# Optimization experiments

Hardware: AMD Instinct MI355X
Metric: run time of the kernel (lower is better)

## Reference

```python
import jax, jax.numpy as jnp
import numpy as np

H = 4096          # hidden_size
NH = 32           # num query heads
NKV = 8           # num kv heads
HD = H // NH      # head_dim = 128
NE = 8            # num_experts
TOPK = 2
ROPE_THETA = 10000.0
EPS = 1e-6


def rmsnorm(x, w):
    var = jnp.mean(x * x, axis=-1, keepdims=True)
    return x * jax.lax.rsqrt(var + EPS) * w


def apply_rope_neox(x, positions):
    # x: [N, heads, HD]; neox style: rotate halves
    half = HD // 2
    inv_freq = 1.0 / (ROPE_THETA ** (jnp.arange(0, HD, 2, dtype=jnp.float32) / HD))  # [half]
    ang = positions.astype(jnp.float32)[:, None] * inv_freq[None, :]                 # [N, half]
    cos = jnp.cos(ang)[:, None, :]  # [N,1,half]
    sin = jnp.sin(ang)[:, None, :]
    x1, x2 = x[..., :half], x[..., half:]
    return jnp.concatenate([x1 * cos - x2 * sin, x2 * cos + x1 * sin], axis=-1)


def setup_inputs() -> dict:
    key = jax.random.key(0)
    ks = jax.random.split(key, 6)
    N = 2048
    return {
        "positions": jnp.arange(N, dtype=jnp.int32),
        "hidden_states": jax.random.normal(ks[0], (N, H), dtype=jnp.float32),
        "w_qkv": jax.random.normal(ks[1], (H, (NH + 2 * NKV) * HD), dtype=jnp.float32) * 0.02,
        "w_o": jax.random.normal(ks[2], (NH * HD, H), dtype=jnp.float32) * 0.02,
        "w_gate": jax.random.normal(ks[3], (H, NE), dtype=jnp.float32) * 0.02,
        "rms_w_pre": jnp.ones((H,), dtype=jnp.float32),
        "rms_w_post": jnp.ones((H,), dtype=jnp.float32),
        "expert_logits": jax.random.uniform(ks[4], (N, NE), dtype=jnp.float32),
    }


def reference(positions, hidden_states, w_qkv, w_o, w_gate, rms_w_pre, rms_w_post, expert_logits):
    N = hidden_states.shape[0]
    # pre-attention RMSNorm (residual is None branch)
    residual = hidden_states
    x = rmsnorm(hidden_states, rms_w_pre)

    qkv = x @ w_qkv
    q = qkv[:, : NH * HD].reshape(N, NH, HD)
    k = qkv[:, NH * HD : (NH + NKV) * HD].reshape(N, NKV, HD)
    v = qkv[:, (NH + NKV) * HD :].reshape(N, NKV, HD)

    q = apply_rope_neox(q, positions)
    k = apply_rope_neox(k, positions)

    # GQA causal self-attention (prefill, single sequence)
    group = NH // NKV
    k_rep = jnp.repeat(k, group, axis=1)  # [N, NH, HD]
    v_rep = jnp.repeat(v, group, axis=1)
    scale = HD ** -0.5
    scores = jnp.einsum("qhd,khd->hqk", q, k_rep) * scale  # [NH, N, N]
    causal = jnp.tril(jnp.ones((N, N), dtype=bool))
    scores = jnp.where(causal[None], scores, jnp.finfo(scores.dtype).min)
    probs = jax.nn.softmax(scores, axis=-1)
    attn_out = jnp.einsum("hqk,khd->qhd", probs, v_rep).reshape(N, NH * HD)

    output = attn_out @ w_o
    # post-attention RMSNorm with fused residual add (vLLM semantics)
    s = output + residual
    residual = s
    output = rmsnorm(s, rms_w_post)

    router_logits = output @ w_gate  # computed as in source; routing result overwritten below

    # random_routing: topk over random expert logits, renormalized
    topk_weights, topk_ids = jax.lax.top_k(expert_logits, TOPK)  # [N, TOPK]
    topk_weights = topk_weights / jnp.sum(topk_weights, axis=-1, keepdims=True)

    # permute_by_exp_ids: stable sort of flattened expert ids, gather tokens
    reorder_ids = jnp.argsort(topk_ids.reshape(-1), stable=True)  # [N*TOPK]
    permuted_output = output[reorder_ids // TOPK]                 # [N*TOPK, H]
    return permuted_output, topk_weights, topk_ids, reorder_ids
```

## Files before the change

kernel.cpp:

```cpp
#include <hip/hip_runtime.h>
#include <hip/hip_bf16.h>
#include <math.h>

#define N_TOK 2048
#define H_DIM 4096
#define NH 32
#define NKV 8
#define HD 128
#define QKV_D 6144
#define NE 8
#define TOPK 2

#define OUT_PERM 0
#define OUT_W    16777216
#define OUT_IDS  16781312
#define OUT_REO  16785408

typedef __bf16 bf16x8 __attribute__((ext_vector_type(8)));
typedef float f32x4 __attribute__((ext_vector_type(4)));

typedef __attribute__((address_space(3))) void lds_void;
typedef __attribute__((address_space(1))) const void gbl_void;

__device__ __forceinline__ void gld16(const void* g, void* l) {
    __builtin_amdgcn_global_load_lds((gbl_void*)g, (lds_void*)l, 16, 0, 0);
}

__device__ __forceinline__ unsigned short f2bf(float f) {
    union { float f; unsigned u; } v; v.f = f;
    unsigned r = v.u + 0x7fff + ((v.u >> 16) & 1);
    return (unsigned short)(r >> 16);
}
__device__ __forceinline__ unsigned pack2bf(float a, float b) {
    return (unsigned)f2bf(a) | ((unsigned)f2bf(b) << 16);
}
__device__ __forceinline__ float bf2f(unsigned short u) {
    union { unsigned u; float f; } v; v.u = ((unsigned)u) << 16;
    return v.f;
}

__global__ __launch_bounds__(256) void rmsnorm_k(const float* __restrict__ x,
                                                 const float* __restrict__ w,
                                                 float* __restrict__ yf,
                                                 unsigned short* __restrict__ yb) {
    int row = blockIdx.x;
    int tid = threadIdx.x;
    const float4* x4 = (const float4*)(x + (size_t)row * H_DIM);
    const float4* w4 = (const float4*)w;
    float4 v[4];
    float ss = 0.f;
#pragma unroll
    for (int k = 0; k < 4; ++k) {
        v[k] = x4[tid + k * 256];
        ss += v[k].x * v[k].x + v[k].y * v[k].y + v[k].z * v[k].z + v[k].w * v[k].w;
    }
#pragma unroll
    for (int off = 32; off; off >>= 1) ss += __shfl_xor(ss, off);
    __shared__ float sacc[4];
    if ((tid & 63) == 0) sacc[tid >> 6] = ss;
    __syncthreads();
    float tot = sacc[0] + sacc[1] + sacc[2] + sacc[3];
    float sc = rsqrtf(tot * (1.0f / H_DIM) + 1e-6f);
#pragma unroll
    for (int k = 0; k < 4; ++k) {
        float4 ww = w4[tid + k * 256];
        float4 o;
        o.x = v[k].x * sc * ww.x;
        o.y = v[k].y * sc * ww.y;
        o.z = v[k].z * sc * ww.z;
        o.w = v[k].w * sc * ww.w;
        if (yf) {
            *(float4*)(yf + (size_t)row * H_DIM + (tid + k * 256) * 4) = o;
        } else {
            uint2 p;
            p.x = pack2bf(o.x, o.y);
            p.y = pack2bf(o.z, o.w);
            *(uint2*)(yb + (size_t)row * H_DIM + (tid + k * 256) * 4) = p;
        }
    }
}

__global__ __launch_bounds__(256) void convT_k(const float* __restrict__ src,
                                               unsigned short* __restrict__ dst,
                                               int R, int C) {
    __shared__ float t[64][68];
    int r0 = blockIdx.y * 64, c0 = blockIdx.x * 64;
    int tid = threadIdx.x;
    int lr = tid >> 4, lc = tid & 15;
#pragma unroll
    for (int it = 0; it < 4; ++it) {
        int r = lr + it * 16;
        float4 v = *(const float4*)(src + (size_t)(r0 + r) * C + c0 + lc * 4);
        *(float4*)&t[r][lc * 4] = v;
    }
    __syncthreads();
#pragma unroll
    for (int it = 0; it < 4; ++it) {
        int cc = lr + it * 16;
        uint2 o;
        o.x = pack2bf(t[lc * 4 + 0][cc], t[lc * 4 + 1][cc]);
        o.y = pack2bf(t[lc * 4 + 2][cc], t[lc * 4 + 3][cc]);
        *(uint2*)(dst + (size_t)(c0 + cc) * R + r0 + lc * 4) = o;
    }
}

__global__ __launch_bounds__(256) void gemm_k(const __hip_bfloat16* __restrict__ A,
                                              const __hip_bfloat16* __restrict__ Bt,
                                              float* __restrict__ C,
                                              unsigned short* __restrict__ Cb,
                                              const float* __restrict__ residual,
                                              int Ncols) {
    __shared__ __align__(16) __hip_bfloat16 As[2][128 * 64];
    __shared__ __align__(16) __hip_bfloat16 Bs[2][128 * 64];
    const int K = H_DIM;
    int tid = threadIdx.x, w = tid >> 6, lane = tid & 63;
    int quad = lane >> 4, l15 = lane & 15;

    int gx = gridDim.x;
    int nwg = gx * gridDim.y;
    int v = blockIdx.y * gx + blockIdx.x;
    int lin = (v & 7) * (nwg >> 3) + (v >> 3);
    int m0 = (lin % gx) * 128, n0 = (lin / gx) * 128;
    int wm = (w & 1) * 64, wn = (w >> 1) * 64;

    int rowInChunk = lane >> 3;
    int uIdx = lane & 7;
    const char* Ag[4]; const char* Bg[4];
    int chOff[4];
#pragma unroll
    for (int c = 0; c < 4; ++c) {
        int ch = w * 4 + c;
        int r = ch * 8 + rowInChunk;
        int gu = uIdx ^ (r & 7);
        Ag[c] = (const char*)(A + (size_t)(m0 + r) * K) + gu * 16;
        Bg[c] = (const char*)(Bt + (size_t)(n0 + r) * K) + gu * 16;
        chOff[c] = ch * 1024;
    }

    f32x4 acc[4][4];
#pragma unroll
    for (int i = 0; i < 4; ++i)
#pragma unroll
        for (int j = 0; j < 4; ++j) acc[i][j] = (f32x4){0.f, 0.f, 0.f, 0.f};

    const int nsteps = K / 64;

#pragma unroll
    for (int c = 0; c < 4; ++c) gld16(Ag[c], (char*)&As[0][0] + chOff[c]);
#pragma unroll
    for (int c = 0; c < 4; ++c) gld16(Bg[c], (char*)&Bs[0][0] + chOff[c]);

    for (int t = 0; t < nsteps; ++t) {
        int cur = t & 1;
        if (t + 1 < nsteps) {
            size_t kb = (size_t)(t + 1) * 128;
            char* dA = (char*)&As[cur ^ 1][0];
            char* dB = (char*)&Bs[cur ^ 1][0];
#pragma unroll
            for (int c = 0; c < 4; ++c) gld16(Ag[c] + kb, dA + chOff[c]);
#pragma unroll
            for (int c = 0; c < 4; ++c) gld16(Bg[c] + kb, dB + chOff[c]);
            asm volatile("s_waitcnt vmcnt(8)" ::: "memory");
        } else {
            asm volatile("s_waitcnt vmcnt(0)" ::: "memory");
        }
        __builtin_amdgcn_sched_barrier(0);
        __builtin_amdgcn_s_barrier();
        __builtin_amdgcn_sched_barrier(0);

        const char* sA = (const char*)&As[cur][0];
        const char* sB = (const char*)&Bs[cur][0];
#pragma unroll
        for (int kk = 0; kk < 2; ++kk) {
            bf16x8 af[4], bfr[4];
#pragma unroll
            for (int mt = 0; mt < 4; ++mt) {
                int m = wm + mt * 16 + l15;
                af[mt] = *(const bf16x8*)(sA + m * 128 + (((kk * 4 + quad) ^ (m & 7)) * 16));
            }
#pragma unroll
            for (int nt = 0; nt < 4; ++nt) {
                int n = wn + nt * 16 + l15;
                bfr[nt] = *(const bf16x8*)(sB + n * 128 + (((kk * 4 + quad) ^ (n & 7)) * 16));
            }
#pragma unroll
            for (int mt = 0; mt < 4; ++mt)
#pragma unroll
                for (int nt = 0; nt < 4; ++nt)
                    acc[mt][nt] = __builtin_amdgcn_mfma_f32_16x16x32_bf16(af[mt], bfr[nt], acc[mt][nt], 0, 0, 0);
        }
        __builtin_amdgcn_sched_barrier(0);
        __builtin_amdgcn_s_barrier();
        __builtin_amdgcn_sched_barrier(0);
    }
#pragma unroll
    for (int mt = 0; mt < 4; ++mt)
#pragma unroll
        for (int nt = 0; nt < 4; ++nt)
#pragma unroll
            for (int r = 0; r < 4; ++r) {
                int row = m0 + wm + mt * 16 + quad * 4 + r;
                int col = n0 + wn + nt * 16 + l15;
                size_t off = (size_t)row * Ncols + col;
                float vv = acc[mt][nt][r];
                if (Cb) {
                    Cb[off] = f2bf(vv);
                } else {
                    if (residual) vv += residual[off];
                    C[off] = vv;
                }
            }
}

__global__ __launch_bounds__(512) void gemm8_k(const __hip_bfloat16* __restrict__ A,
                                               const __hip_bfloat16* __restrict__ Bt,
                                               unsigned short* __restrict__ Cb,
                                               int Ncols) {
    __shared__ __align__(16) __hip_bfloat16 As[2][256 * 64];
    __shared__ __align__(16) __hip_bfloat16 Bs[2][256 * 64];
    const int K = H_DIM;
    int tid = threadIdx.x, w = tid >> 6, lane = tid & 63;
    int quad = lane >> 4, l15 = lane & 15;
    int wr = w >> 2, wc = w & 3;

    int gx = gridDim.x;
    int nwg = gx * gridDim.y;
    int v = blockIdx.y * gx + blockIdx.x;
    int lin = (v & 7) * (nwg >> 3) + (v >> 3);
    int m0 = (lin % gx) * 256, n0 = (lin / gx) * 256;

    const char* Abase = (const char*)A + (size_t)m0 * (K * 2);
    const char* Bbase = (const char*)Bt + (size_t)n0 * (K * 2);
    int srow = w * 8 + (lane >> 3);

    auto stage = [&](const char* gbase, int rowoff, char* lbase, size_t kbyte) {
#pragma unroll
        for (int l = 0; l < 2; ++l) {
            int r = l * 64 + srow;
            int gu = (lane & 7) ^ (r & 7);
            gld16(gbase + (size_t)(rowoff + r) * (K * 2) + kbyte + gu * 16,
                  lbase + (l * 64 + w * 8) * 128);
        }
    };

    f32x4 acc[8][4];
#pragma unroll
    for (int i = 0; i < 8; ++i)
#pragma unroll
        for (int j = 0; j < 4; ++j) acc[i][j] = (f32x4){0.f, 0.f, 0.f, 0.f};

    const int ntiles = K / 64;

    stage(Abase, 0,   (char*)&As[0][0],         0);
    stage(Abase, 128, (char*)&As[0][0] + 16384, 0);
    stage(Bbase, 0,   (char*)&Bs[0][0],         0);
    stage(Bbase, 128, (char*)&Bs[0][0] + 16384, 0);
    stage(Bbase, 0,   (char*)&Bs[1][0],         128);
    stage(Bbase, 128, (char*)&Bs[1][0] + 16384, 128);
    asm volatile("s_waitcnt vmcnt(4)" ::: "memory");
    __builtin_amdgcn_sched_barrier(0);
    __builtin_amdgcn_s_barrier();
    __builtin_amdgcn_sched_barrier(0);

    for (int j = 0; j < ntiles; ++j) {
        int d = j & 1;
        const char* sA = (const char*)&As[d][0];
        const char* sB = (const char*)&Bs[d][0];
        char* nA = (char*)&As[d ^ 1][0];
        char* pB = (char*)&Bs[d][0];
        size_t kb1 = (size_t)(j + 1) * 128, kb2 = (size_t)(j + 2) * 128;
        bf16x8 aR[4][2], bR[4][2];

#pragma unroll
        for (int mt = 0; mt < 4; ++mt)
#pragma unroll
            for (int kk = 0; kk < 2; ++kk) {
                int m = wr * 128 + mt * 16 + l15;
                aR[mt][kk] = *(const bf16x8*)(sA + m * 128 + (((kk * 4 + quad) ^ (m & 7)) * 16));
            }
#pragma unroll
        for (int nt = 0; nt < 2; ++nt)
#pragma unroll
            for (int kk = 0; kk < 2; ++kk) {
                int n = wc * 64 + nt * 16 + l15;
                bR[nt][kk] = *(const bf16x8*)(sB + n * 128 + (((kk * 4 + quad) ^ (n & 7)) * 16));
            }
        if (j + 1 < ntiles) stage(Abase, 0, nA, kb1);
        __builtin_amdgcn_sched_barrier(0);
        __builtin_amdgcn_s_barrier();
        asm volatile("s_waitcnt lgkmcnt(0)" ::: "memory");
        __builtin_amdgcn_sched_barrier(0);
        __builtin_amdgcn_s_setprio(1);
#pragma unroll
        for (int mt = 0; mt < 4; ++mt)
#pragma unroll
            for (int nt = 0; nt < 2; ++nt)
#pragma unroll
                for (int kk = 0; kk < 2; ++kk)
                    acc[mt][nt] = __builtin_amdgcn_mfma_f32_16x16x32_bf16(aR[mt][kk], bR[nt][kk], acc[mt][nt], 0, 0, 0);
        __builtin_amdgcn_s_setprio(0);
        __builtin_amdgcn_sched_barrier(0);
        __builtin_amdgcn_s_barrier();
        __builtin_amdgcn_sched_barrier(0);

#pragma unroll
        for (int nt = 2; nt < 4; ++nt)
#pragma unroll
            for (int kk = 0; kk < 2; ++kk) {
                int n = wc * 64 + nt * 16 + l15;
                bR[nt][kk] = *(const bf16x8*)(sB + n * 128 + (((kk * 4 + quad) ^ (n & 7)) * 16));
            }
        if (j + 1 < ntiles) stage(Abase, 128, nA + 16384, kb1);
        __builtin_amdgcn_sched_barrier(0);
        __builtin_amdgcn_s_barrier();
        asm volatile("s_waitcnt lgkmcnt(0)" ::: "memory");
        __builtin_amdgcn_sched_barrier(0);
        __builtin_amdgcn_s_setprio(1);
#pragma unroll
        for (int mt = 0; mt < 4; ++mt)
#pragma unroll
            for (int nt = 2; nt < 4; ++nt)
#pragma unroll
                for (int kk = 0; kk < 2; ++kk)
                    acc[mt][nt] = __builtin_amdgcn_mfma_f32_16x16x32_bf16(aR[mt][kk], bR[nt][kk], acc[mt][nt], 0, 0, 0);
        __builtin_amdgcn_s_setprio(0);
        __builtin_amdgcn_sched_barrier(0);
        __builtin_amdgcn_s_barrier();
        __builtin_amdgcn_sched_barrier(0);

#pragma unroll
        for (int mt = 0; mt < 4; ++mt)
#pragma unroll
            for (int kk = 0; kk < 2; ++kk) {
                int m = wr * 128 + (mt + 4) * 16 + l15;
                aR[mt][kk] = *(const bf16x8*)(sA + m * 128 + (((kk * 4 + quad) ^ (m & 7)) * 16));
            }
        if (j + 2 < ntiles) stage(Bbase, 0, pB, kb2);
        __builtin_amdgcn_sched_barrier(0);
        __builtin_amdgcn_s_barrier();
        asm volatile("s_waitcnt lgkmcnt(0)" ::: "memory");
        __builtin_amdgcn_sched_barrier(0);
        __builtin_amdgcn_s_setprio(1);
#pragma unroll
        for (int mt = 0; mt < 4; ++mt)
#pragma unroll
            for (int nt = 0; nt < 2; ++nt)
#pragma unroll
                for (int kk = 0; kk < 2; ++kk)
                    acc[mt + 4][nt] = __builtin_amdgcn_mfma_f32_16x16x32_bf16(aR[mt][kk], bR[nt][kk], acc[mt + 4][nt], 0, 0, 0);
        __builtin_amdgcn_s_setprio(0);
        __builtin_amdgcn_sched_barrier(0);
        __builtin_amdgcn_s_barrier();
        __builtin_amdgcn_sched_barrier(0);

        if (j + 2 < ntiles) {
            stage(Bbase, 128, pB + 16384, kb2);
            asm volatile("s_waitcnt vmcnt(4)" ::: "memory");
        } else {
            asm volatile("s_waitcnt vmcnt(0)" ::: "memory");
        }
        __builtin_amdgcn_sched_barrier(0);
        __builtin_amdgcn_s_barrier();
        __builtin_amdgcn_sched_barrier(0);
        __builtin_amdgcn_s_setprio(1);
#pragma unroll
        for (int mt = 0; mt < 4; ++mt)
#pragma unroll
            for (int nt = 2; nt < 4; ++nt)
#pragma unroll
                for (int kk = 0; kk < 2; ++kk)
                    acc[mt + 4][nt] = __builtin_amdgcn_mfma_f32_16x16x32_bf16(aR[mt][kk], bR[nt][kk], acc[mt + 4][nt], 0, 0, 0);
        __builtin_amdgcn_s_setprio(0);
        __builtin_amdgcn_sched_barrier(0);
        __builtin_amdgcn_s_barrier();
        __builtin_amdgcn_sched_barrier(0);
    }

#pragma unroll
    for (int mt = 0; mt < 8; ++mt)
#pragma unroll
        for (int nt = 0; nt < 4; ++nt)
#pragma unroll
            for (int r = 0; r < 4; ++r) {
                int row = m0 + wr * 128 + mt * 16 + quad * 4 + r;
                int col = n0 + wc * 64 + nt * 16 + l15;
                Cb[(size_t)row * Ncols + col] = f2bf(acc[mt][nt][r]);
            }
}

__global__ __launch_bounds__(256) void prep_k(const unsigned short* __restrict__ qkvb,
                                              const int* __restrict__ pos,
                                              unsigned short* __restrict__ Qc,
                                              unsigned short* __restrict__ Kc) {
    int row = blockIdx.x, tid = threadIdx.x;
    float fpos = (float)pos[row];
    const float scale = 0.08838834764831845f;
    const float lg = 0.20762050593045f;
#pragma unroll
    for (int it = 0; it < 8; ++it) {
        int pi = tid + it * 256;
        int head = pi >> 6, t = pi & 63;
        float inv = exp2f(-(float)t * lg);
        float ang = fpos * inv;
        float s = __sinf(ang), c = __cosf(ang);
        const unsigned short* bp = qkvb + (size_t)row * QKV_D + head * HD + t;
        float x1 = bf2f(bp[0]), x2 = bf2f(bp[64]);
        unsigned short* qb = Qc + (size_t)row * H_DIM + head * HD + t;
        qb[0]  = f2bf((x1 * c - x2 * s) * scale);
        qb[64] = f2bf((x2 * c + x1 * s) * scale);
    }
#pragma unroll
    for (int it = 0; it < 2; ++it) {
        int pi = tid + it * 256;
        int kvh = pi >> 6, t = pi & 63;
        float inv = exp2f(-(float)t * lg);
        float ang = fpos * inv;
        float s = __sinf(ang), c = __cosf(ang);
        const unsigned short* bp = qkvb + (size_t)row * QKV_D + H_DIM + kvh * HD + t;
        float x1 = bf2f(bp[0]), x2 = bf2f(bp[64]);
        unsigned short* kb = Kc + ((size_t)kvh * N_TOK + row) * HD + t;
        kb[0]  = f2bf(x1 * c - x2 * s);
        kb[64] = f2bf(x2 * c + x1 * s);
    }
}

__global__ __launch_bounds__(256) void vt_k(const unsigned short* __restrict__ qkvb,
                                            unsigned short* __restrict__ Vt) {
    __shared__ unsigned short ts[64][136];
    int j0 = blockIdx.x * 64, kvh = blockIdx.y, tid = threadIdx.x;
#pragma unroll
    for (int it = 0; it < 4; ++it) {
        int idx = tid + it * 256;
        int r = idx >> 4, c8 = idx & 15;
        *(uint4*)&ts[r][c8 * 8] =
            *(const uint4*)(qkvb + (size_t)(j0 + r) * QKV_D + (NH + NKV) * HD + kvh * HD + c8 * 8);
    }
    __syncthreads();
    int d = tid >> 1, half = tid & 1;
    unsigned short* dst = Vt + ((size_t)kvh * HD + d) * N_TOK + j0 + half * 32;
#pragma unroll
    for (int g = 0; g < 4; ++g) {
        int kb = half * 32 + g * 8;
        uint4 o;
        o.x = (unsigned)ts[kb + 0][d] | ((unsigned)ts[kb + 1][d] << 16);
        o.y = (unsigned)ts[kb + 2][d] | ((unsigned)ts[kb + 3][d] << 16);
        o.z = (unsigned)ts[kb + 4][d] | ((unsigned)ts[kb + 5][d] << 16);
        o.w = (unsigned)ts[kb + 6][d] | ((unsigned)ts[kb + 7][d] << 16);
        *(uint4*)(dst + g * 8) = o;
    }
}

__global__ __launch_bounds__(512) void attn_k(const __hip_bfloat16* __restrict__ Qc,
                                              const __hip_bfloat16* __restrict__ Kc,
                                              const __hip_bfloat16* __restrict__ Vt,
                                              unsigned short* __restrict__ ao) {
    __shared__ __align__(16) __hip_bfloat16 Ks[2][32 * 128];
    __shared__ __align__(16) __hip_bfloat16 Vs[2][128 * 32];
    __shared__ __align__(16) unsigned short Pw[8][16 * 40];

    int tid = threadIdx.x, w = tid >> 6, lane = tid & 63;
    int quad = lane >> 4, l15 = lane & 15;
    int pr = blockIdx.y;
    int kvh = pr >> 1;
    int h = kvh * 4 + (pr & 1) * 2 + (w & 1);
    int qt = gridDim.x - 1 - blockIdx.x;
    int i0 = qt * 64;
    int i0q = i0 + (w >> 1) * 16;
    int q = i0q + l15;

    bf16x8 qf[4];
    const __hip_bfloat16* qrow = Qc + (size_t)q * H_DIM + h * HD;
#pragma unroll
    for (int kf = 0; kf < 4; ++kf)
        qf[kf] = *(const bf16x8*)(qrow + kf * 32 + quad * 8);

    const char* KcH = (const char*)(Kc + (size_t)kvh * N_TOK * HD);
    const char* VtH = (const char*)(Vt + (size_t)kvh * HD * N_TOK);

    int kKey = w * 4 + (lane >> 4);
    int kPart = (lane & 15) ^ (kKey & 15);
    int vD = w * 16 + (lane >> 2);
    int vP = (lane & 3) ^ (vD & 3);
    char* Kl[2] = { (char*)&Ks[0][0] + w * 1024, (char*)&Ks[1][0] + w * 1024 };
    char* Vl[2] = { (char*)&Vs[0][0] + w * 1024, (char*)&Vs[1][0] + w * 1024 };

    float mstat = -INFINITY, lstat = 0.f;
    f32x4 o[8];
#pragma unroll
    for (int nt = 0; nt < 8; ++nt) o[nt] = (f32x4){0.f, 0.f, 0.f, 0.f};

    int nsteps = (i0 + 64) >> 5;

    gld16(KcH + (size_t)kKey * 256 + kPart * 16, Kl[0]);
    gld16(VtH + (size_t)vD * (N_TOK * 2) + vP * 16, Vl[0]);
    __syncthreads();

    for (int t = 0; t < nsteps; ++t) {
        int j0 = t << 5;
        int cur = t & 1;
        if (t + 1 < nsteps) {
            int jn = j0 + 32;
            gld16(KcH + (size_t)(jn + kKey) * 256 + kPart * 16, Kl[cur ^ 1]);
            gld16(VtH + (size_t)vD * (N_TOK * 2) + (size_t)jn * 2 + vP * 16, Vl[cur ^ 1]);
        }
        if (j0 <= i0q + 15) {
            const char* Kb = (const char*)&Ks[cur][0];
            const char* Vb = (const char*)&Vs[cur][0];

            f32x4 s[2];
            s[0] = (f32x4){0.f, 0.f, 0.f, 0.f};
            s[1] = (f32x4){0.f, 0.f, 0.f, 0.f};
#pragma unroll
            for (int mt = 0; mt < 2; ++mt) {
                int key = mt * 16 + l15;
#pragma unroll
                for (int kf = 0; kf < 4; ++kf) {
                    bf16x8 kfr = *(const bf16x8*)(Kb + key * 256 + (((kf * 4 + quad) ^ (key & 15)) * 16));
                    s[mt] = __builtin_amdgcn_mfma_f32_16x16x32_bf16(kfr, qf[kf], s[mt], 0, 0, 0);
                }
            }
            if (j0 + 31 > i0q) {
#pragma unroll
                for (int mt = 0; mt < 2; ++mt) {
                    int keyb = j0 + mt * 16 + quad * 4;
#pragma unroll
                    for (int r = 0; r < 4; ++r)
                        if (keyb + r > q) s[mt][r] = -INFINITY;
                }
            }
            float mx = fmaxf(fmaxf(fmaxf(s[0][0], s[0][1]), fmaxf(s[0][2], s[0][3])),
                             fmaxf(fmaxf(s[1][0], s[1][1]), fmaxf(s[1][2], s[1][3])));
            mx = fmaxf(mx, __shfl_xor(mx, 16));
            mx = fmaxf(mx, __shfl_xor(mx, 32));
            float newm = fmaxf(mstat, mx);
            float alpha = __expf(mstat - newm);
            float p[8];
#pragma unroll
            for (int mt = 0; mt < 2; ++mt)
#pragma unroll
                for (int r = 0; r < 4; ++r) p[mt * 4 + r] = __expf(s[mt][r] - newm);
            float ps = p[0] + p[1] + p[2] + p[3] + p[4] + p[5] + p[6] + p[7];
            ps += __shfl_xor(ps, 16);
            ps += __shfl_xor(ps, 32);
            lstat = lstat * alpha + ps;
            mstat = newm;

            unsigned* pwb = (unsigned*)(&Pw[w][0]);
            int eo = l15 * 20 + quad * 2;
            pwb[eo]     = pack2bf(p[0], p[1]);
            pwb[eo + 1] = pack2bf(p[2], p[3]);
            pwb[eo + 8] = pack2bf(p[4], p[5]);
            pwb[eo + 9] = pack2bf(p[6], p[7]);
            bf16x8 pf = *(const bf16x8*)(&Pw[w][l15 * 40 + quad * 8]);

            float alq[4];
#pragma unroll
            for (int r = 0; r < 4; ++r) alq[r] = __shfl(alpha, quad * 4 + r);
#pragma unroll
            for (int nt = 0; nt < 8; ++nt)
#pragma unroll
                for (int r = 0; r < 4; ++r) o[nt][r] *= alq[r];

#pragma unroll
            for (int nt = 0; nt < 8; ++nt) {
                int d = nt * 16 + l15;
                bf16x8 vf = *(const bf16x8*)(Vb + d * 64 + ((quad ^ (d & 3)) * 16));
                o[nt] = __builtin_amdgcn_mfma_f32_16x16x32_bf16(pf, vf, o[nt], 0, 0, 0);
            }
        }
        __syncthreads();
    }

    float linv[4];
#pragma unroll
    for (int r = 0; r < 4; ++r) linv[r] = 1.f / __shfl(lstat, quad * 4 + r);
#pragma unroll
    for (int nt = 0; nt < 8; ++nt)
#pragma unroll
        for (int r = 0; r < 4; ++r) {
            int row = i0q + quad * 4 + r;
            int col = h * HD + nt * 16 + l15;
            ao[(size_t)row * H_DIM + col] = f2bf(o[nt][r] * linv[r]);
        }
}

__global__ __launch_bounds__(256) void topk_k(const float* __restrict__ elog,
                                              float* __restrict__ w_out,
                                              float* __restrict__ id_out,
                                              int* __restrict__ ids_int) {
    int row = blockIdx.x * 256 + threadIdx.x;
    if (row >= N_TOK) return;
    const float4* e4 = (const float4*)(elog + (size_t)row * NE);
    float4 a = e4[0], b = e4[1];
    float e[8] = {a.x, a.y, a.z, a.w, b.x, b.y, b.z, b.w};
    int id0 = 0;
    float b0 = e[0];
#pragma unroll
    for (int t = 1; t < 8; ++t)
        if (e[t] > b0) { b0 = e[t]; id0 = t; }
    int id1 = -1;
    float b1 = -INFINITY;
#pragma unroll
    for (int t = 0; t < 8; ++t)
        if (t != id0 && e[t] > b1) { b1 = e[t]; id1 = t; }
    float s = b0 + b1;
    w_out[row * 2 + 0] = b0 / s;
    w_out[row * 2 + 1] = b1 / s;
    id_out[row * 2 + 0] = (float)id0;
    id_out[row * 2 + 1] = (float)id1;
    ids_int[row * 2 + 0] = id0;
    ids_int[row * 2 + 1] = id1;
}

__global__ __launch_bounds__(256) void sort_k(const int* __restrict__ ids,
                                              float* __restrict__ reorder_out,
                                              int* __restrict__ perm) {
    __shared__ int sh[N_TOK * TOPK];
    int tid = threadIdx.x;
    for (int r = tid; r < N_TOK * TOPK; r += 256) sh[r] = ids[r];
    __syncthreads();
    int i = blockIdx.x * 256 + tid;
    int e = sh[i];
    int rank = 0;
    for (int j = 0; j < N_TOK * TOPK; ++j) {
        int ej = sh[j];
        rank += (ej < e) ? 1 : ((ej == e && j < i) ? 1 : 0);
    }
    reorder_out[rank] = (float)i;
    perm[rank] = i;
}

__global__ __launch_bounds__(256) void gather_k(const float* __restrict__ src,
                                                const int* __restrict__ perm,
                                                float* __restrict__ dst) {
    int r = blockIdx.x;
    int srow = perm[r] >> 1;
    const float4* s4 = (const float4*)(src + (size_t)srow * H_DIM);
    float4* d4 = (float4*)(dst + (size_t)r * H_DIM);
    int tid = threadIdx.x;
#pragma unroll
    for (int k = 0; k < 4; ++k) d4[tid + k * 256] = s4[tid + k * 256];
}

extern "C" void kernel_launch(void* const* d_in, const int* in_sizes, int n_in,
                              void* d_out, int out_size, void* d_ws, size_t ws_size,
                              hipStream_t stream) {
    const int*   positions = (const int*)d_in[0];
    const float* hidden    = (const float*)d_in[1];
    const float* w_qkv     = (const float*)d_in[2];
    const float* w_o       = (const float*)d_in[3];
    const float* rms_pre   = (const float*)d_in[5];
    const float* rms_post  = (const float*)d_in[6];
    const float* elog      = (const float*)d_in[7];
    float* out = (float*)d_out;

    char* ws = (char*)d_ws;
    unsigned short* wqkvT = (unsigned short*)(ws);
    unsigned short* woT   = (unsigned short*)(ws);
    float*          post  = (float*)(ws + 33554432ULL);
    unsigned short* xn    = (unsigned short*)(ws + 50331648ULL);
    unsigned short* aout  = (unsigned short*)(ws + 50331648ULL);
    unsigned short* qkvb  = (unsigned short*)(ws + 67108864ULL);
    float*          sbuf  = (float*)(ws + 67108864ULL);
    unsigned short* Qc    = (unsigned short*)(ws + 117440512ULL);
    unsigned short* Kc    = (unsigned short*)(ws + 134217728ULL);
    unsigned short* Vt    = (unsigned short*)(ws + 138412032ULL);
    int* ids_int  = (int*)(ws + 142606336ULL);
    int* perm_int = (int*)(ws + 142622720ULL);

    convT_k<<<dim3(QKV_D / 64, H_DIM / 64), 256, 0, stream>>>(w_qkv, wqkvT, H_DIM, QKV_D);
    rmsnorm_k<<<N_TOK, 256, 0, stream>>>(hidden, rms_pre, nullptr, xn);
    gemm8_k<<<dim3(N_TOK / 256, QKV_D / 256), 512, 0, stream>>>(
        (const __hip_bfloat16*)xn, (const __hip_bfloat16*)wqkvT, qkvb, QKV_D);
    convT_k<<<dim3(H_DIM / 64, H_DIM / 64), 256, 0, stream>>>(w_o, woT, H_DIM, H_DIM);
    prep_k<<<N_TOK, 256, 0, stream>>>(qkvb, positions, Qc, Kc);
    vt_k<<<dim3(N_TOK / 64, NKV), 256, 0, stream>>>(qkvb, Vt);
    attn_k<<<dim3(N_TOK / 64, 16), 512, 0, stream>>>(
        (const __hip_bfloat16*)Qc, (const __hip_bfloat16*)Kc, (const __hip_bfloat16*)Vt, aout);
    gemm_k<<<dim3(N_TOK / 128, H_DIM / 128), 256, 0, stream>>>(
        (const __hip_bfloat16*)aout, (const __hip_bfloat16*)woT, sbuf, nullptr, hidden, H_DIM);
    rmsnorm_k<<<N_TOK, 256, 0, stream>>>(sbuf, rms_post, post, nullptr);
    topk_k<<<N_TOK / 256, 256, 0, stream>>>(elog, out + OUT_W, out + OUT_IDS, ids_int);
    sort_k<<<(N_TOK * TOPK) / 256, 256, 0, stream>>>(ids_int, out + OUT_REO, perm_int);
    gather_k<<<N_TOK * TOPK, 256, 0, stream>>>(post, perm_int, out + OUT_PERM);
}
```

Measured before the change: 717.3 us.

## Collapse GEMM main loop from four barrier phases to two

Merges the four sub-phases of the bf16 MFMA GEMM k-loop into two. Each phase now loads all four B fragments, issues both halves of the next A or B tile stage together, and runs a 4x4 MFMA block. This removes several s_barrier and lgkmcnt waits per k-tile, cutting synchronization stalls and allowing more MFMA work between barriers. In exchange, more fragment registers are live at once, and global loads are issued in larger bursts with less interleaving against compute.

Result: no change. 714.5 us (-0.4%).

```diff
diff --git a/kernel.cpp b/kernel.cpp
--- a/kernel.cpp
+++ b/kernel.cpp
@@ -279,22 +279,21 @@
                 aR[mt][kk] = *(const bf16x8*)(sA + m * 128 + (((kk * 4 + quad) ^ (m & 7)) * 16));
             }
 #pragma unroll
-        for (int nt = 0; nt < 2; ++nt)
+        for (int nt = 0; nt < 4; ++nt)
 #pragma unroll
             for (int kk = 0; kk < 2; ++kk) {
                 int n = wc * 64 + nt * 16 + l15;
                 bR[nt][kk] = *(const bf16x8*)(sB + n * 128 + (((kk * 4 + quad) ^ (n & 7)) * 16));
             }
-        if (j + 1 < ntiles) stage(Abase, 0, nA, kb1);
-        __builtin_amdgcn_sched_barrier(0);
-        __builtin_amdgcn_s_barrier();
-        asm volatile("s_waitcnt lgkmcnt(0)" ::: "memory");
-        __builtin_amdgcn_sched_barrier(0);
+        if (j + 1 < ntiles) {
+            stage(Abase, 0,   nA,         kb1);
+            stage(Abase, 128, nA + 16384, kb1);
+        }
         __builtin_amdgcn_s_setprio(1);
 #pragma unroll
         for (int mt = 0; mt < 4; ++mt)
 #pragma unroll
-            for (int nt = 0; nt < 2; ++nt)
+            for (int nt = 0; nt < 4; ++nt)
 #pragma unroll
                 for (int kk = 0; kk < 2; ++kk)
                     acc[mt][nt] = __builtin_amdgcn_mfma_f32_16x16x32_bf16(aR[mt][kk], bR[nt][kk], acc[mt][nt], 0, 0, 0);
@@ -304,73 +303,30 @@
         __builtin_amdgcn_sched_barrier(0);
 
 #pragma unroll
-        for (int nt = 2; nt < 4; ++nt)
-#pragma unroll
-            for (int kk = 0; kk < 2; ++kk) {
-                int n = wc * 64 + nt * 16 + l15;
-                bR[nt][kk] = *(const bf16x8*)(sB + n * 128 + (((kk * 4 + quad) ^ (n & 7)) * 16));
-            }
-        if (j + 1 < ntiles) stage(Abase, 128, nA + 16384, kb1);
-        __builtin_amdgcn_sched_barrier(0);
-        __builtin_amdgcn_s_barrier();
-        asm volatile("s_waitcnt lgkmcnt(0)" ::: "memory");
-        __builtin_amdgcn_sched_barrier(0);
-        __builtin_amdgcn_s_setprio(1);
-#pragma unroll
-        for (int mt = 0; mt < 4; ++mt)
-#pragma unroll
-            for (int nt = 2; nt < 4; ++nt)
-#pragma unroll
-                for (int kk = 0; kk < 2; ++kk)
-                    acc[mt][nt] = __builtin_amdgcn_mfma_f32_16x16x32_bf16(aR[mt][kk], bR[nt][kk], acc[mt][nt], 0, 0, 0);
-        __builtin_amdgcn_s_setprio(0);
-        __builtin_amdgcn_sched_barrier(0);
-        __builtin_amdgcn_s_barrier();
-        __builtin_amdgcn_sched_barrier(0);
-
-#pragma unroll
         for (int mt = 0; mt < 4; ++mt)
 #pragma unroll
             for (int kk = 0; kk < 2; ++kk) {
                 int m = wr * 128 + (mt + 4) * 16 + l15;
                 aR[mt][kk] = *(const bf16x8*)(sA + m * 128 + (((kk * 4 + quad) ^ (m & 7)) * 16));
             }
-        if (j + 2 < ntiles) stage(Bbase, 0, pB, kb2);
-        __builtin_amdgcn_sched_barrier(0);
-        __builtin_amdgcn_s_barrier();
-        asm volatile("s_waitcnt lgkmcnt(0)" ::: "memory");
-        __builtin_amdgcn_sched_barrier(0);
+        if (j + 2 < ntiles) {
+            stage(Bbase, 0,   pB,         kb2);
+            stage(Bbase, 128, pB + 16384, kb2);
+        }
         __builtin_amdgcn_s_setprio(1);
 #pragma unroll
         for (int mt = 0; mt < 4; ++mt)
 #pragma unroll
-            for (int nt = 0; nt < 2; ++nt)
+            for (int nt = 0; nt < 4; ++nt)
 #pragma unroll
                 for (int kk = 0; kk < 2; ++kk)
                     acc[mt + 4][nt] = __builtin_amdgcn_mfma_f32_16x16x32_bf16(aR[mt][kk], bR[nt][kk], acc[mt + 4][nt], 0, 0, 0);
         __builtin_amdgcn_s_setprio(0);
-        __builtin_amdgcn_sched_barrier(0);
-        __builtin_amdgcn_s_barrier();
-        __builtin_amdgcn_sched_barrier(0);
-
         if (j + 2 < ntiles) {
-            stage(Bbase, 128, pB + 16384, kb2);
             asm volatile("s_waitcnt vmcnt(4)" ::: "memory");
         } else {
             asm volatile("s_waitcnt vmcnt(0)" ::: "memory");
         }
-        __builtin_amdgcn_sched_barrier(0);
-        __builtin_amdgcn_s_barrier();
-        __builtin_amdgcn_sched_barrier(0);
-        __builtin_amdgcn_s_setprio(1);
-#pragma unroll
-        for (int mt = 0; mt < 4; ++mt)
-#pragma unroll
-            for (int nt = 2; nt < 4; ++nt)
-#pragma unroll
-                for (int kk = 0; kk < 2; ++kk)
-                    acc[mt + 4][nt] = __builtin_amdgcn_mfma_f32_16x16x32_bf16(aR[mt][kk], bR[nt][kk], acc[mt + 4][nt], 0, 0, 0);
-        __builtin_amdgcn_s_setprio(0);
         __builtin_amdgcn_sched_barrier(0);
         __builtin_amdgcn_s_barrier();
         __builtin_amdgcn_sched_barrier(0);
```
